# Performance work log

Measured on AMD Instinct MI355X. Metric: run time of the kernel, lower is better.

Reference implementation:

```python
import jax, jax.numpy as jnp
import numpy as np

HEADS = 8
SR = 2
EPS_BN = 1e-5
EPS_LN = 1e-5


def _conv(x, w, b, stride=1, pad=0):
    y = jax.lax.conv_general_dilated(x, w, (stride, stride), [(pad, pad), (pad, pad)],
                                     dimension_numbers=('NCHW', 'OIHW', 'NCHW'))
    return y + b[None, :, None, None]


def _bn(x, g, b):
    # eval-mode BatchNorm with running_mean=0, running_var=1
    return x * (g / jnp.sqrt(1.0 + EPS_BN))[None, :, None, None] + b[None, :, None, None]


def _dwt_haar(x):
    # [B,c,H,W] -> [B,4c,H/2,W/2] stacked as LL,HL,LH,HH (Wave-ViT convention)
    x1 = x[:, :, 0::2, 0::2] / 2
    x2 = x[:, :, 1::2, 0::2] / 2
    x3 = x[:, :, 0::2, 1::2] / 2
    x4 = x[:, :, 1::2, 1::2] / 2
    ll = x1 + x2 + x3 + x4
    hl = -x1 - x2 + x3 + x4
    lh = -x1 + x2 - x3 + x4
    hh = x1 - x2 - x3 + x4
    return jnp.concatenate([ll, hl, lh, hh], axis=1)


def _idwt_haar(y):
    # [B,4c,h,w] -> [B,c,2h,2w], exact inverse of _dwt_haar
    c = y.shape[1] // 4
    ll, hl, lh, hh = y[:, :c], y[:, c:2 * c], y[:, 2 * c:3 * c], y[:, 3 * c:]
    p1 = (ll - hl - lh + hh) / 2  # (0::2, 0::2)
    p2 = (ll - hl + lh - hh) / 2  # (1::2, 0::2)
    p3 = (ll + hl - lh - hh) / 2  # (0::2, 1::2)
    p4 = (ll + hl + lh + hh) / 2  # (1::2, 1::2)
    B, _, h2, w2 = ll.shape
    row0 = jnp.stack([p1, p3], axis=-1)  # even rows
    row1 = jnp.stack([p2, p4], axis=-1)  # odd rows
    out = jnp.stack([row0, row1], axis=3)  # [B,c,h2,2,w2,2]
    return out.reshape(B, c, 2 * h2, 2 * w2)


def setup_inputs() -> dict:
    key = jax.random.key(0)
    ks = jax.random.split(key, 12)
    B, H, W, C = 8, 56, 56, 512
    N = H * W
    c4 = C // 4

    def nrm(k, shp, std):
        return jax.random.normal(k, shp, jnp.float32) * std

    return {
        'x': jax.random.normal(ks[0], (B, N, C), jnp.float32),
        'H': H, 'W': W,
        'reduce_w': nrm(ks[1], (c4, C, 1, 1), (2.0 / c4) ** 0.5),
        'reduce_b': jnp.zeros((c4,), jnp.float32),
        'reduce_g': jnp.ones((c4,), jnp.float32),
        'reduce_beta': jnp.zeros((c4,), jnp.float32),
        'filter_w': nrm(ks[2], (C, C, 3, 3), (2.0 / (9 * C)) ** 0.5),
        'filter_b': jnp.zeros((C,), jnp.float32),
        'filter_g': jnp.ones((C,), jnp.float32),
        'filter_beta': jnp.zeros((C,), jnp.float32),
        'q_w': nrm(ks[3], (C, C), 0.02),
        'q_b': jnp.zeros((C,), jnp.float32),
        'ln_g': jnp.ones((C,), jnp.float32),
        'ln_b': jnp.zeros((C,), jnp.float32),
        'kv_w': nrm(ks[4], (2 * C, C), 0.02),
        'kv_b': jnp.zeros((2 * C,), jnp.float32),
        'kve_w': nrm(ks[5], (C, C, SR, SR), (2.0 / (SR * SR * C)) ** 0.5),
        'kve_b': jnp.zeros((C,), jnp.float32),
        'proj_w': nrm(ks[6], (C, C + c4), 0.02),
        'proj_b': jnp.zeros((C,), jnp.float32),
    }


def reference(x, H, W, reduce_w, reduce_b, reduce_g, reduce_beta,
              filter_w, filter_b, filter_g, filter_beta,
              q_w, q_b, ln_g, ln_b, kv_w, kv_b, kve_w, kve_b, proj_w, proj_b):
    B, N, C = x.shape
    hd = C // HEADS
    scale = hd ** -0.5

    q = (x @ q_w.T + q_b).reshape(B, N, HEADS, hd).transpose(0, 2, 1, 3)  # [B,h,N,d]

    xi = x.reshape(B, H, W, C).transpose(0, 3, 1, 2)  # NCHW
    r = jax.nn.relu(_bn(_conv(xi, reduce_w, reduce_b), reduce_g, reduce_beta))  # [B,C/4,H,W]
    r16 = r.astype(jnp.float16)
    x_dwt = _dwt_haar(r16).astype(jnp.float32)  # [B,C,H/2,W/2]
    x_dwt = jax.nn.relu(_bn(_conv(x_dwt, filter_w, filter_b, pad=1), filter_g, filter_beta))
    x_dwt16 = x_dwt.astype(jnp.float16)
    x_idwt = _idwt_haar(x_dwt16)  # [B,C/4,H,W] fp16
    x_idwt = x_idwt.reshape(B, C // 4, H * W).transpose(0, 2, 1)  # [B,N,C/4]

    x_dwt = x_dwt16.astype(jnp.float32)
    kv_in = _conv(x_dwt, kve_w, kve_b, stride=SR).reshape(B, C, -1).transpose(0, 2, 1)  # [B,M,C]
    mu = kv_in.mean(-1, keepdims=True)
    var = ((kv_in - mu) ** 2).mean(-1, keepdims=True)
    kv_n = (kv_in - mu) / jnp.sqrt(var + EPS_LN) * ln_g + ln_b
    kv = (kv_n @ kv_w.T + kv_b).reshape(B, -1, 2, HEADS, hd).transpose(2, 0, 3, 1, 4)
    k, v = kv[0], kv[1]  # [B,h,M,d]

    attn = jax.nn.softmax(jnp.einsum('bhnd,bhmd->bhnm', q, k) * scale, axis=-1)
    o = jnp.einsum('bhnm,bhmd->bhnd', attn, v).transpose(0, 2, 1, 3).reshape(B, N, C)
    o = jnp.concatenate([o, x_idwt.astype(jnp.float32)], axis=-1)  # [B,N,C+C/4]
    return o @ proj_w.T + proj_b
```

## Files before the change

kernel.cpp:

```cpp
#include <hip/hip_runtime.h>
#include <math.h>


typedef _Float16 half8 __attribute__((ext_vector_type(8)));
typedef float f32x4 __attribute__((ext_vector_type(4)));

static const size_t OFF_X16  = 0;
static const size_t OFF_Q16  = 12845056;
static const size_t OFF_CAT  = 25690112;
static const size_t OFF_R16  = 41746432;
static const size_t OFF_PAD  = 44957696;
static const size_t OFF_DWTB = 48644096;
static const size_t OFF_QRW  = 51855360;
static const size_t OFF_LN16 = 55066624;
static const size_t OFF_KV16 = 55869440;
static const size_t OFF_WT   = 57475072;
static const size_t OFF_KT   = 59834368;
static const size_t OFF_KVW  = 61145088;
static const size_t OFF_PW   = 61669376;
static const size_t OFF_VT   = 62062592;
static const size_t OFF_PART = 62980096;

#define BN_RSQ 0.9999950000374997f
#define SCL2   0.1803368801111204f
#define PART_STRIDE 3211264
#define KVE_STRIDE  802816

__device__ __forceinline__ void async_copy16(const _Float16* g, _Float16* l) {
    __builtin_amdgcn_global_load_lds(
        (const __attribute__((address_space(1))) void*)g,
        (__attribute__((address_space(3))) void*)l, 16, 0, 0);
}

#define WAIT4_BARRIER() asm volatile("s_waitcnt vmcnt(4)\n\ts_barrier" ::: "memory")
#define WAIT0_BARRIER() asm volatile("s_waitcnt vmcnt(0)\n\ts_barrier" ::: "memory")

template <int ALOAD, int EPI>
__global__ __launch_bounds__(256) void gemm16(
    const _Float16* __restrict__ A, const _Float16* __restrict__ W,
    void* __restrict__ outp, int M, int K, int lda, int ldc,
    const float* __restrict__ bias, const float* __restrict__ bng,
    const float* __restrict__ bnb, const float* __restrict__ bias2,
    void* __restrict__ outp2)
{
    __shared__ _Float16 sA[3][128 * 32];
    __shared__ _Float16 sB[3][128 * 32];
    const int t = threadIdx.x;
    const int lane = t & 63, wid = t >> 6;

    int bx = blockIdx.x, by = blockIdx.y;
    {
        int nwg = gridDim.x * gridDim.y;
        if ((nwg & 7) == 0) {
            int orig = by * gridDim.x + bx;
            int cs = nwg >> 3;
            int wg = (orig & 7) * cs + (orig >> 3);
            by = wg % gridDim.y;
            bx = wg / gridDim.y;
        }
    }
    const int m0 = bx * 128, n0 = by * 128;
    const int kbase = blockIdx.z * K;

    const int sr = wid * 16 + (lane >> 2);
    const int sc = (lane & 3) * 8;
    const int stA0 = wid * 512;
    const int stA1 = 2048 + wid * 512;

    const _Float16 *aP0, *aP1;
    if constexpr (ALOAD == 0) {
        int r0 = m0 + sr;      if (r0 > M - 1) r0 = M - 1;
        int r1 = m0 + 64 + sr; if (r1 > M - 1) r1 = M - 1;
        aP0 = A + (size_t)r0 * lda + sc;
        aP1 = A + (size_t)r1 * lda + sc;
    } else {
        int m_ = m0 + sr; if (m_ > M - 1) m_ = M - 1;
        int b_ = m_ / 196, rem = m_ - b_ * 196, i_ = rem / 14, j_ = rem - i_ * 14;
        aP0 = A + ((size_t)(b_ * 784 + 2 * i_ * 28 + 2 * j_)) * 512 + sc;
        m_ = m0 + 64 + sr; if (m_ > M - 1) m_ = M - 1;
        b_ = m_ / 196; rem = m_ - b_ * 196; i_ = rem / 14; j_ = rem - i_ * 14;
        aP1 = A + ((size_t)(b_ * 784 + 2 * i_ * 28 + 2 * j_)) * 512 + sc;
    }
    const int ldw = (ALOAD == 2) ? lda : K;
    const _Float16* bP0 = W + (size_t)(n0 + sr) * ldw + sc;
    const _Float16* bP1 = W + (size_t)(n0 + 64 + sr) * ldw + sc;

    const int mw = wid & 1, nw = wid >> 1;
    const int pAoff = (mw * 64 + (lane & 15)) * 32 + (lane >> 4) * 8;
    const int pBoff = (nw * 64 + (lane & 15)) * 32 + (lane >> 4) * 8;

    f32x4 acc[4][4];
#pragma unroll
    for (int i = 0; i < 4; ++i)
#pragma unroll
        for (int j = 0; j < 4; ++j) acc[i][j] = (f32x4)(0.0f);

    auto aoff_of = [&](int k) -> int {
        if constexpr (ALOAD == 0) {
            return k;
        } else {
            int sub = k >> 9; int ky = sub >> 1, kx = sub & 1;
            return (ky * 28 + kx) * 512 + (k & 511);
        }
    };
    auto stage = [&](int ti, int buf) {
        int k = kbase + ti * 32;
        int aOff = aoff_of(k);
        async_copy16(aP0 + aOff, &sA[buf][stA0]);
        async_copy16(aP1 + aOff, &sA[buf][stA1]);
        async_copy16(bP0 + k, &sB[buf][stA0]);
        async_copy16(bP1 + k, &sB[buf][stA1]);
    };

    const int nt = K >> 5;
    stage(0, 0);
    if (nt > 1) { stage(1, 1); WAIT4_BARRIER(); }
    else        { WAIT0_BARRIER(); }

    int cur = 0;
    for (int i = 0; i < nt; ++i) {
        const _Float16* pA = &sA[cur][0] + pAoff;
        const _Float16* pB = &sB[cur][0] + pBoff;
        half8 aF[4], bF[4];
#pragma unroll
        for (int u = 0; u < 4; ++u) aF[u] = *(const half8*)(pA + u * 512);
#pragma unroll
        for (int u = 0; u < 4; ++u) bF[u] = *(const half8*)(pB + u * 512);

        const bool st = (i + 2 < nt);
        if (st) {
            int nb = cur + 2; if (nb >= 3) nb -= 3;
            stage(i + 2, nb);
        }
#pragma unroll
        for (int u = 0; u < 4; ++u)
#pragma unroll
            for (int j = 0; j < 4; ++j)
                acc[u][j] = __builtin_amdgcn_mfma_f32_16x16x32_f16(
                    aF[u], bF[j], acc[u][j], 0, 0, 0);

        if (i + 1 < nt) {
            if (st) WAIT4_BARRIER();
            else    WAIT0_BARRIER();
        }
        ++cur; if (cur == 3) cur = 0;
    }

    const int orow = m0 + mw * 64 + (lane >> 4) * 4;
    const int ocol = n0 + nw * 64 + (lane & 15);
#pragma unroll
    for (int j = 0; j < 4; ++j) {
        int col = ocol + j * 16;
        float bv = 0.0f, g = 0.0f, b2 = 0.0f;
        if constexpr (EPI == 4) {
            if (n0 >= 512) {
                bv = bias2[col - 512];
                g = bng[col - 512] * BN_RSQ;
                b2 = bnb[col - 512];
            } else {
                bv = bias[col];
            }
        } else if constexpr (EPI != 3) {
            bv = bias[col];
        }
#pragma unroll
        for (int i = 0; i < 4; ++i) {
#pragma unroll
            for (int r = 0; r < 4; ++r) {
                int row = orow + i * 16 + r;
                if (row >= M) continue;
                float v = acc[i][j][r] + bv;
                if constexpr (EPI == 0) {
                    __builtin_nontemporal_store(
                        v, (float*)outp + (size_t)row * ldc + col);
                } else if constexpr (EPI == 3) {
                    ((float*)outp)[(size_t)blockIdx.z * KVE_STRIDE
                                   + (size_t)row * ldc + col] = v;
                } else if constexpr (EPI == 4) {
                    if (n0 >= 512) {
                        v = fmaxf(v * g + b2, 0.0f);
                        ((_Float16*)outp2)[(size_t)row * 128 + (col - 512)] =
                            (_Float16)v;
                    } else {
                        ((_Float16*)outp)[(size_t)row * ldc + col] = (_Float16)v;
                    }
                } else if constexpr (EPI == 5) {
                    if (n0 >= 512) {
                        int hd_ = col - 512;
                        int h_ = hd_ >> 6, d_ = hd_ & 63;
                        int b_ = row / 196, m_ = row - b_ * 196;
                        ((_Float16*)outp2)[((size_t)((b_ * 8 + h_) * 64 + d_)) * 224
                                           + m_] = (_Float16)v;
                    } else {
                        ((_Float16*)outp)[(size_t)row * ldc + col] = (_Float16)v;
                    }
                } else {
                    ((_Float16*)outp)[(size_t)row * ldc + col] = (_Float16)v;
                }
            }
        }
    }
}

__global__ __launch_bounds__(256) void conv_splitk(
    const _Float16* __restrict__ A, const _Float16* __restrict__ W,
    float* __restrict__ partA, float* __restrict__ partB)
{
    __shared__ _Float16 sA[3][128 * 32];
    __shared__ _Float16 sB[3][128 * 32];
    const int t = threadIdx.x;
    const int lane = t & 63, wid = t >> 6;

    int orig = blockIdx.x;
    int wg = (orig & 7) * 98 + (orig >> 3);
    int bx = wg % 49;  int c = wg / 49;
    int by = c & 3,    bz = c >> 2;

    const int m0 = bx * 128, n0 = by * 128;
    const int kbase = bz * 1152;

    const int sr = wid * 16 + (lane >> 2);
    const int sc = (lane & 3) * 8;
    const int stA0 = wid * 512;
    const int stA1 = 2048 + wid * 512;

    int m_ = m0 + sr;
    int b_ = m_ / 784, rem = m_ - b_ * 784, y_ = rem / 28, x_ = rem - y_ * 28;
    const _Float16* aP0 = A + ((size_t)(b_ * 900 + (y_ + 1) * 30 + (x_ + 1))) * 512 + sc;
    m_ = m0 + 64 + sr;
    b_ = m_ / 784; rem = m_ - b_ * 784; y_ = rem / 28; x_ = rem - y_ * 28;
    const _Float16* aP1 = A + ((size_t)(b_ * 900 + (y_ + 1) * 30 + (x_ + 1))) * 512 + sc;
    const _Float16* bP0 = W + (size_t)(n0 + sr) * 4608 + sc;
    const _Float16* bP1 = W + (size_t)(n0 + 64 + sr) * 4608 + sc;

    const int mw = wid & 1, nw = wid >> 1;
    const int pAoff = (mw * 64 + (lane & 15)) * 32 + (lane >> 4) * 8;
    const int pBoff = (nw * 64 + (lane & 15)) * 32 + (lane >> 4) * 8;

    f32x4 acc[4][4];
#pragma unroll
    for (int i = 0; i < 4; ++i)
#pragma unroll
        for (int j = 0; j < 4; ++j) acc[i][j] = (f32x4)(0.0f);

    auto aoff_of = [&](int k) -> int {
        int sub = k >> 9; int s3 = sub / 3;
        int dy = s3 - 1, dx = sub - s3 * 3 - 1;
        return (dy * 30 + dx) * 512 + (k & 511);
    };
    auto stage = [&](int ti, int buf) {
        int k = kbase + ti * 32;
        int aOff = aoff_of(k);
        async_copy16(aP0 + aOff, &sA[buf][stA0]);
        async_copy16(aP1 + aOff, &sA[buf][stA1]);
        async_copy16(bP0 + k, &sB[buf][stA0]);
        async_copy16(bP1 + k, &sB[buf][stA1]);
    };

    const int nt = 36;
    stage(0, 0);
    stage(1, 1);
    WAIT4_BARRIER();

    int cur = 0;
    for (int i = 0; i < nt; ++i) {
        const _Float16* pA = &sA[cur][0] + pAoff;
        const _Float16* pB = &sB[cur][0] + pBoff;
        half8 aF[4], bF[4];
#pragma unroll
        for (int u = 0; u < 4; ++u) aF[u] = *(const half8*)(pA + u * 512);
#pragma unroll
        for (int u = 0; u < 4; ++u) bF[u] = *(const half8*)(pB + u * 512);

        const bool st = (i + 2 < nt);
        if (st) {
            int nb = cur + 2; if (nb >= 3) nb -= 3;
            stage(i + 2, nb);
        }
#pragma unroll
        for (int u = 0; u < 4; ++u)
#pragma unroll
            for (int j = 0; j < 4; ++j)
                acc[u][j] = __builtin_amdgcn_mfma_f32_16x16x32_f16(
                    aF[u], bF[j], acc[u][j], 0, 0, 0);

        if (i + 1 < nt) {
            if (st) WAIT4_BARRIER();
            else    WAIT0_BARRIER();
        }
        ++cur; if (cur == 3) cur = 0;
    }

    float* dst = (bz < 2) ? (partA + (size_t)bz * PART_STRIDE)
                          : (partB + (size_t)(bz - 2) * PART_STRIDE);
    const int orow = m0 + mw * 64 + (lane >> 4) * 4;
    const int ocol = n0 + nw * 64 + (lane & 15);
#pragma unroll
    for (int j = 0; j < 4; ++j) {
#pragma unroll
        for (int i = 0; i < 4; ++i)
#pragma unroll
            for (int r = 0; r < 4; ++r)
                dst[(size_t)(orow + i * 16 + r) * 512 + ocol + j * 16] = acc[i][j][r];
    }
}

__global__ __launch_bounds__(128) void conv_epi_idwt(
    const float* __restrict__ pA, const float* __restrict__ pB,
    _Float16* __restrict__ dwtb, _Float16* __restrict__ cat,
    const float* __restrict__ bias, const float* __restrict__ bng,
    const float* __restrict__ bnb)
{
    int p = blockIdx.x;
    int b = p / 784; int rem = p - b * 784;
    int i = rem / 28;  int j = rem - i * 28;
    int c = threadIdx.x;
    size_t base = (size_t)p * 512;
    _Float16 g16[4];
#pragma unroll
    for (int g = 0; g < 4; ++g) {
        int ch = g * 128 + c;
        float s = (pA[base + ch] + pA[PART_STRIDE + base + ch])
                + (pB[base + ch] + pB[PART_STRIDE + base + ch]);
        float v = (s + bias[ch]) * (bng[ch] * BN_RSQ) + bnb[ch];
        g16[g] = (_Float16)fmaxf(v, 0.0f);
        dwtb[base + ch] = g16[g];
    }
    _Float16 ll = g16[0], hl = g16[1], lh = g16[2], hh = g16[3];
    _Float16 h = (_Float16)0.5f;
    _Float16 p1 = (((ll - hl) - lh) + hh) * h;
    _Float16 p2 = (((ll - hl) + lh) - hh) * h;
    _Float16 p3 = (((ll + hl) - lh) - hh) * h;
    _Float16 p4 = (((ll + hl) + lh) + hh) * h;
    int y = 2 * i, x = 2 * j;
    size_t rb = (size_t)b * 3136;
    __builtin_nontemporal_store(p1, &cat[(rb + (size_t)y * 56 + x) * 640 + 512 + c]);
    __builtin_nontemporal_store(p3, &cat[(rb + (size_t)y * 56 + x + 1) * 640 + 512 + c]);
    __builtin_nontemporal_store(p2, &cat[(rb + (size_t)(y + 1) * 56 + x) * 640 + 512 + c]);
    __builtin_nontemporal_store(p4, &cat[(rb + (size_t)(y + 1) * 56 + x + 1) * 640 + 512 + c]);
}

__device__ __forceinline__ void cvt8_at(
    const float* __restrict__ s, _Float16* __restrict__ d, int i)
{
    const float4* sp = (const float4*)(s + (size_t)i * 8);
    float4 a = sp[0], b = sp[1];
    half8 h;
    h[0] = (_Float16)a.x; h[1] = (_Float16)a.y; h[2] = (_Float16)a.z; h[3] = (_Float16)a.w;
    h[4] = (_Float16)b.x; h[5] = (_Float16)b.y; h[6] = (_Float16)b.z; h[7] = (_Float16)b.w;
    *(half8*)(d + (size_t)i * 8) = h;
}

__global__ __launch_bounds__(256) void prep_kernel(
    const float* __restrict__ qw, const float* __restrict__ rw,
    const float* __restrict__ kvw, const float* __restrict__ pw,
    const float* __restrict__ fw, const float* __restrict__ kw,
    _Float16* __restrict__ qrw16, _Float16* __restrict__ kvw16,
    _Float16* __restrict__ pw16, _Float16* __restrict__ wT,
    _Float16* __restrict__ kT, _Float16* __restrict__ pad,
    _Float16* __restrict__ vt)
{
    int bid = blockIdx.x, tid = threadIdx.x;
    if (bid < 128) {
        cvt8_at(qw, qrw16, bid * 256 + tid);
    } else if (bid < 160) {
        cvt8_at(rw, qrw16 + 262144, (bid - 128) * 256 + tid);
    } else if (bid < 416) {
        cvt8_at(kvw, kvw16, (bid - 160) * 256 + tid);
    } else if (bid < 576) {
        cvt8_at(pw, pw16, (bid - 416) * 256 + tid);
    } else if (bid < 9792) {
        int idx = (bid - 576) * 256 + tid;
        int n = idx / 4608; int r = idx - n * 4608;
        int sub = r >> 9; int ci = r & 511;
        wT[idx] = (_Float16)fw[(size_t)n * 4608 + ci * 9 + sub];
    } else if (bid < 13888) {
        int idx = (bid - 9792) * 256 + tid;
        int n = idx >> 11; int r = idx & 2047;
        int sub = r >> 9; int ci = r & 511;
        kT[idx] = (_Float16)kw[((size_t)n << 11) + (ci << 2) + sub];
    } else if (bid < 15688) {
        int i = (bid - 13888) * 256 + tid;
        *(float4*)(pad + (size_t)i * 8) = make_float4(0.f, 0.f, 0.f, 0.f);
    } else {
        int i = (bid - 15688) * 256 + tid;
        *(float4*)(vt + (size_t)i * 8) = make_float4(0.f, 0.f, 0.f, 0.f);
    }
}

__global__ __launch_bounds__(256) void cvt_f32_f16(
    const float* __restrict__ s, _Float16* __restrict__ d, int n8)
{
    int i = blockIdx.x * 256 + threadIdx.x;
    if (i >= n8) return;
    cvt8_at(s, d, i);
}

__global__ __launch_bounds__(128) void dwt_kernel(
    const _Float16* __restrict__ r, _Float16* __restrict__ pad)
{
    int bid = blockIdx.x;
    int b = bid / 784; int rem = bid - b * 784;
    int i = rem / 28;  int j = rem - i * 28;
    int c = threadIdx.x;
    int y = 2 * i, x = 2 * j;
    size_t base = (size_t)b * 3136;
    _Float16 f1 = r[(base + (size_t)y * 56 + x) * 128 + c];
    _Float16 f2 = r[(base + (size_t)(y + 1) * 56 + x) * 128 + c];
    _Float16 f3 = r[(base + (size_t)y * 56 + (x + 1)) * 128 + c];
    _Float16 f4 = r[(base + (size_t)(y + 1) * 56 + (x + 1)) * 128 + c];
    _Float16 h = (_Float16)0.5f;
    _Float16 x1 = f1 * h, x2 = f2 * h, x3 = f3 * h, x4 = f4 * h;
    _Float16 ll = ((x1 + x2) + x3) + x4;
    _Float16 hl = (((-x1) - x2) + x3) + x4;
    _Float16 lh = (((-x1) + x2) - x3) + x4;
    _Float16 hh = ((x1 - x2) - x3) + x4;
    size_t ob = ((size_t)b * 900 + (size_t)(i + 1) * 30 + (j + 1)) * 512;
    pad[ob + c]       = ll;
    pad[ob + 128 + c] = hl;
    pad[ob + 256 + c] = lh;
    pad[ob + 384 + c] = hh;
}

__global__ __launch_bounds__(256) void ln_kernel(
    const float* __restrict__ part, _Float16* __restrict__ o,
    const float* __restrict__ g, const float* __restrict__ bta,
    const float* __restrict__ kvb)
{
    int wave = threadIdx.x >> 6;
    int lane = threadIdx.x & 63;
    int row = blockIdx.x * 4 + wave;
    int c = lane * 8;
    const float* rp = part + (size_t)row * 512 + c;
    float v[8];
#pragma unroll
    for (int i = 0; i < 8; i += 4) {
        float4 a0 = *(const float4*)(rp + i);
        float4 a1 = *(const float4*)(rp + KVE_STRIDE + i);
        float4 a2 = *(const float4*)(rp + 2 * KVE_STRIDE + i);
        float4 a3 = *(const float4*)(rp + 3 * KVE_STRIDE + i);
        v[i + 0] = (a0.x + a1.x) + (a2.x + a3.x) + kvb[c + i + 0];
        v[i + 1] = (a0.y + a1.y) + (a2.y + a3.y) + kvb[c + i + 1];
        v[i + 2] = (a0.z + a1.z) + (a2.z + a3.z) + kvb[c + i + 2];
        v[i + 3] = (a0.w + a1.w) + (a2.w + a3.w) + kvb[c + i + 3];
    }
    float s = ((v[0] + v[1]) + (v[2] + v[3])) + ((v[4] + v[5]) + (v[6] + v[7]));
#pragma unroll
    for (int off = 32; off; off >>= 1) s += __shfl_xor(s, off);
    float mu = s * (1.0f / 512.0f);
    float sq = 0.0f;
#pragma unroll
    for (int i = 0; i < 8; ++i) { v[i] -= mu; sq += v[i] * v[i]; }
#pragma unroll
    for (int off = 32; off; off >>= 1) sq += __shfl_xor(sq, off);
    float inv = 1.0f / sqrtf(sq * (1.0f / 512.0f) + 1e-5f);
    half8 hv;
#pragma unroll
    for (int i = 0; i < 8; ++i) hv[i] = (_Float16)(v[i] * inv * g[c + i] + bta[c + i]);
    *(half8*)(o + (size_t)row * 512 + c) = hv;
}

__global__ __launch_bounds__(256) void attn_mfma(
    const _Float16* __restrict__ q, const _Float16* __restrict__ kv,
    const _Float16* __restrict__ vt, _Float16* __restrict__ cat)
{
    __shared__ _Float16 sK[64][72];
    __shared__ _Float16 sVT[64][72];
    __shared__ _Float16 sP[4][16][40];
    int bid = blockIdx.x;
    int qt = bid % 49;
    int h  = (bid / 49) & 7;
    int b  = bid / 392;
    int n0 = qt * 64;
    int t = threadIdx.x, lane = t & 63, wid = t >> 6;
    int quad = lane >> 4, l16 = lane & 15;

    const _Float16* qp = q + ((size_t)(b * 3136 + n0 + wid * 16 + l16)) * 512
                           + h * 64 + quad * 8;
    half8 aQ0 = *(const half8*)qp;
    half8 aQ1 = *(const half8*)(qp + 32);

    f32x4 oacc[4];
#pragma unroll
    for (int i = 0; i < 4; ++i) oacc[i] = (f32x4)(0.0f);
    float lsum[4] = {0.f, 0.f, 0.f, 0.f};

    const _Float16* vtb = vt + ((size_t)((b * 8 + h) * 64)) * 224;

    for (int c0 = 0; c0 < 224; c0 += 64) {
        __syncthreads();
#pragma unroll
        for (int it = 0; it < 2; ++it) {
            int slot = t + 256 * it;
            int row = slot >> 3, c8 = (slot & 7) * 8;
            int m = c0 + row; if (m > 195) m = 195;
            *(half8*)&sK[row][c8] =
                *(const half8*)(kv + ((size_t)(b * 196 + m)) * 1024 + h * 64 + c8);
        }
#pragma unroll
        for (int it = 0; it < 2; ++it) {
            int slot = t + 256 * it;
            int row = slot >> 3, c8 = (slot & 7) * 8;
            *(half8*)&sVT[row][c8] =
                *(const half8*)(vtb + (size_t)row * 224 + c0 + c8);
        }
        __syncthreads();

#pragma unroll
        for (int sc = 0; sc < 64; sc += 32) {
            half8 bk00 = *(const half8*)&sK[sc + l16][quad * 8];
            half8 bk01 = *(const half8*)&sK[sc + l16][32 + quad * 8];
            half8 bk10 = *(const half8*)&sK[sc + 16 + l16][quad * 8];
            half8 bk11 = *(const half8*)&sK[sc + 16 + l16][32 + quad * 8];
            f32x4 s0 = (f32x4)(0.0f), s1 = (f32x4)(0.0f);
            s0 = __builtin_amdgcn_mfma_f32_16x16x32_f16(aQ0, bk00, s0, 0, 0, 0);
            s0 = __builtin_amdgcn_mfma_f32_16x16x32_f16(aQ1, bk01, s0, 0, 0, 0);
            s1 = __builtin_amdgcn_mfma_f32_16x16x32_f16(aQ0, bk10, s1, 0, 0, 0);
            s1 = __builtin_amdgcn_mfma_f32_16x16x32_f16(aQ1, bk11, s1, 0, 0, 0);

            int col0 = c0 + sc + l16;
            float msk0 = (col0 < 196) ? 0.0f : -INFINITY;
            float msk1 = (col0 + 16 < 196) ? 0.0f : -INFINITY;
            float p0[4], p1[4];
#pragma unroll
            for (int r = 0; r < 4; ++r) {
                p0[r] = exp2f(s0[r] * SCL2 + msk0);
                p1[r] = exp2f(s1[r] * SCL2 + msk1);
                lsum[r] += p0[r] + p1[r];
            }
#pragma unroll
            for (int r = 0; r < 4; ++r) {
                sP[wid][quad * 4 + r][l16]      = (_Float16)p0[r];
                sP[wid][quad * 4 + r][16 + l16] = (_Float16)p1[r];
            }
            half8 aP = *(const half8*)&sP[wid][l16][quad * 8];
            half8 bv0 = *(const half8*)&sVT[l16][sc + quad * 8];
            half8 bv1 = *(const half8*)&sVT[16 + l16][sc + quad * 8];
            half8 bv2 = *(const half8*)&sVT[32 + l16][sc + quad * 8];
            half8 bv3 = *(const half8*)&sVT[48 + l16][sc + quad * 8];
            oacc[0] = __builtin_amdgcn_mfma_f32_16x16x32_f16(aP, bv0, oacc[0], 0, 0, 0);
            oacc[1] = __builtin_amdgcn_mfma_f32_16x16x32_f16(aP, bv1, oacc[1], 0, 0, 0);
            oacc[2] = __builtin_amdgcn_mfma_f32_16x16x32_f16(aP, bv2, oacc[2], 0, 0, 0);
            oacc[3] = __builtin_amdgcn_mfma_f32_16x16x32_f16(aP, bv3, oacc[3], 0, 0, 0);
        }
    }

    float inv[4];
#pragma unroll
    for (int r = 0; r < 4; ++r) {
        float s = lsum[r];
        s += __shfl_xor(s, 1);
        s += __shfl_xor(s, 2);
        s += __shfl_xor(s, 4);
        s += __shfl_xor(s, 8);
        inv[r] = 1.0f / s;
    }
#pragma unroll
    for (int r = 0; r < 4; ++r) {
        size_t rowoff = ((size_t)(b * 3136 + n0 + wid * 16 + quad * 4 + r)) * 640
                        + h * 64 + l16;
#pragma unroll
        for (int tv = 0; tv < 4; ++tv)
            cat[rowoff + tv * 16] = (_Float16)(oacc[tv][r] * inv[r]);
    }
}

extern "C" void kernel_launch(void* const* d_in, const int* in_sizes, int n_in,
                              void* d_out, int out_size, void* d_ws, size_t ws_size,
                              hipStream_t stream)
{
    const float* x           = (const float*)d_in[0];
    const float* reduce_w    = (const float*)d_in[3];
    const float* reduce_b    = (const float*)d_in[4];
    const float* reduce_g    = (const float*)d_in[5];
    const float* reduce_beta = (const float*)d_in[6];
    const float* filter_w    = (const float*)d_in[7];
    const float* filter_b    = (const float*)d_in[8];
    const float* filter_g    = (const float*)d_in[9];
    const float* filter_beta = (const float*)d_in[10];
    const float* q_w         = (const float*)d_in[11];
    const float* q_b         = (const float*)d_in[12];
    const float* ln_g        = (const float*)d_in[13];
    const float* ln_b        = (const float*)d_in[14];
    const float* kv_w        = (const float*)d_in[15];
    const float* kv_b        = (const float*)d_in[16];
    const float* kve_w       = (const float*)d_in[17];
    const float* kve_b       = (const float*)d_in[18];
    const float* proj_w      = (const float*)d_in[19];
    const float* proj_b      = (const float*)d_in[20];
    float* out = (float*)d_out;
    _Float16* hws = (_Float16*)d_ws;

    _Float16* x16    = hws + OFF_X16;
    _Float16* q16    = hws + OFF_Q16;
    _Float16* cat16  = hws + OFF_CAT;
    _Float16* r16    = hws + OFF_R16;
    _Float16* pad16  = hws + OFF_PAD;
    _Float16* dwtb16 = hws + OFF_DWTB;
    _Float16* qrw16  = hws + OFF_QRW;
    _Float16* ln16   = hws + OFF_LN16;
    _Float16* kv16   = hws + OFF_KV16;
    _Float16* wT16   = hws + OFF_WT;
    _Float16* kT16   = hws + OFF_KT;
    _Float16* kvw16  = hws + OFF_KVW;
    _Float16* pw16   = hws + OFF_PW;
    _Float16* vt16   = hws + OFF_VT;
    float*    partA  = (float*)(hws + OFF_X16);
    float*    partB  = (float*)(hws + OFF_PART);
    float*    kvepart = (float*)(hws + OFF_X16);

    prep_kernel<<<dim3(16136), dim3(256), 0, stream>>>(
        q_w, reduce_w, kv_w, proj_w, filter_w, kve_w,
        qrw16, kvw16, pw16, wT16, kT16, pad16, vt16);

    cvt_f32_f16<<<dim3(6272), dim3(256), 0, stream>>>(x, x16, 1605632);

    gemm16<0, 4><<<dim3(196, 5), dim3(256), 0, stream>>>(
        x16, qrw16, q16, 25088, 512, 512, 512, q_b, reduce_g, reduce_beta,
        reduce_b, r16);

    dwt_kernel<<<dim3(6272), dim3(128), 0, stream>>>(r16, pad16);

    conv_splitk<<<dim3(784), dim3(256), 0, stream>>>(pad16, wT16, partA, partB);

    conv_epi_idwt<<<dim3(6272), dim3(128), 0, stream>>>(
        partA, partB, dwtb16, cat16, filter_b, filter_g, filter_beta);

    gemm16<2, 3><<<dim3(13, 4, 4), dim3(256), 0, stream>>>(
        dwtb16, kT16, kvepart, 1568, 512, 2048, 512, nullptr, nullptr, nullptr,
        nullptr, nullptr);

    ln_kernel<<<dim3(392), dim3(256), 0, stream>>>(kvepart, ln16, ln_g, ln_b, kve_b);

    gemm16<0, 5><<<dim3(13, 8), dim3(256), 0, stream>>>(
        ln16, kvw16, kv16, 1568, 512, 512, 1024, kv_b, nullptr, nullptr,
        nullptr, vt16);

    attn_mfma<<<dim3(3136), dim3(256), 0, stream>>>(q16, kv16, vt16, cat16);

    gemm16<0, 0><<<dim3(196, 4), dim3(256), 0, stream>>>(
        cat16, pw16, out, 25088, 640, 640, 512, proj_b, nullptr, nullptr,
        nullptr, nullptr);
}
```

Measured before the change: 399.0 us.

## Use 256x128 tiles for large GEMMs and conv; fuse x conversion into prep

Adds a gemm16f variant and a conv_splitk_fat kernel that compute 256x128 output tiles per block (8x4 MFMA accumulators per wave) instead of 128x128. The QR, proj GEMMs and the 3x3 conv now run on these, halving grid size and doubling A-tile reuse of each B tile. The f32-to-f16 conversion of x is folded into prep_kernel to save a launch. The larger tiles raise register and LDS use, which can lower occupancy, and leave fewer blocks to fill the GPU (400 for the conv).

```diff
diff --git a/kernel.cpp b/kernel.cpp
--- a/kernel.cpp
+++ b/kernel.cpp
@@ -33,15 +33,14 @@
 }
 
 #define WAIT4_BARRIER() asm volatile("s_waitcnt vmcnt(4)\n\ts_barrier" ::: "memory")
+#define WAIT6_BARRIER() asm volatile("s_waitcnt vmcnt(6)\n\ts_barrier" ::: "memory")
 #define WAIT0_BARRIER() asm volatile("s_waitcnt vmcnt(0)\n\ts_barrier" ::: "memory")
 
 template <int ALOAD, int EPI>
 __global__ __launch_bounds__(256) void gemm16(
     const _Float16* __restrict__ A, const _Float16* __restrict__ W,
     void* __restrict__ outp, int M, int K, int lda, int ldc,
-    const float* __restrict__ bias, const float* __restrict__ bng,
-    const float* __restrict__ bnb, const float* __restrict__ bias2,
-    void* __restrict__ outp2)
+    const float* __restrict__ bias, void* __restrict__ outp2)
 {
     __shared__ _Float16 sA[3][128 * 32];
     __shared__ _Float16 sB[3][128 * 32];
@@ -49,16 +48,6 @@
     const int lane = t & 63, wid = t >> 6;
 
     int bx = blockIdx.x, by = blockIdx.y;
-    {
-        int nwg = gridDim.x * gridDim.y;
-        if ((nwg & 7) == 0) {
-            int orig = by * gridDim.x + bx;
-            int cs = nwg >> 3;
-            int wg = (orig & 7) * cs + (orig >> 3);
-            by = wg % gridDim.y;
-            bx = wg / gridDim.y;
-        }
-    }
     const int m0 = bx * 128, n0 = by * 128;
     const int kbase = blockIdx.z * K;
 
@@ -151,6 +140,131 @@
 #pragma unroll
     for (int j = 0; j < 4; ++j) {
         int col = ocol + j * 16;
+        float bv = 0.0f;
+        if constexpr (EPI == 5) bv = bias[col];
+#pragma unroll
+        for (int i = 0; i < 4; ++i) {
+#pragma unroll
+            for (int r = 0; r < 4; ++r) {
+                int row = orow + i * 16 + r;
+                if (row >= M) continue;
+                float v = acc[i][j][r] + bv;
+                if constexpr (EPI == 3) {
+                    ((float*)outp)[(size_t)blockIdx.z * KVE_STRIDE
+                                   + (size_t)row * ldc + col] = v;
+                } else {
+                    if (n0 >= 512) {
+                        int hd_ = col - 512;
+                        int h_ = hd_ >> 6, d_ = hd_ & 63;
+                        int b_ = row / 196, m_ = row - b_ * 196;
+                        ((_Float16*)outp2)[((size_t)((b_ * 8 + h_) * 64 + d_)) * 224
+                                           + m_] = (_Float16)v;
+                    } else {
+                        ((_Float16*)outp)[(size_t)row * ldc + col] = (_Float16)v;
+                    }
+                }
+            }
+        }
+    }
+}
+
+template <int EPI>
+__global__ __launch_bounds__(256) void gemm16f(
+    const _Float16* __restrict__ A, const _Float16* __restrict__ W,
+    void* __restrict__ outp, int M, int K, int lda, int ldc,
+    const float* __restrict__ bias, const float* __restrict__ bng,
+    const float* __restrict__ bnb, const float* __restrict__ bias2,
+    void* __restrict__ outp2)
+{
+    __shared__ _Float16 sA[3][256 * 32];
+    __shared__ _Float16 sB[3][128 * 32];
+    const int t = threadIdx.x;
+    const int lane = t & 63, wid = t >> 6;
+
+    int bx = blockIdx.x, by = blockIdx.y;
+    {
+        int nwg = gridDim.x * gridDim.y;
+        if ((nwg & 7) == 0) {
+            int orig = by * gridDim.x + bx;
+            int cs = nwg >> 3;
+            int wg = (orig & 7) * cs + (orig >> 3);
+            by = wg % gridDim.y;
+            bx = wg / gridDim.y;
+        }
+    }
+    const int m0 = bx * 256, n0 = by * 128;
+
+    const int sr = wid * 16 + (lane >> 2);
+    const int sc = (lane & 3) * 8;
+    const int stO = wid * 512;
+
+    const _Float16* aP[4];
+#pragma unroll
+    for (int g = 0; g < 4; ++g) {
+        int r_ = m0 + g * 64 + sr; if (r_ > M - 1) r_ = M - 1;
+        aP[g] = A + (size_t)r_ * lda + sc;
+    }
+    const _Float16* bP0 = W + (size_t)(n0 + sr) * K + sc;
+    const _Float16* bP1 = W + (size_t)(n0 + 64 + sr) * K + sc;
+
+    const int mw = wid & 1, nw = wid >> 1;
+    const int pAoff = (mw * 128 + (lane & 15)) * 32 + (lane >> 4) * 8;
+    const int pBoff = (nw * 64 + (lane & 15)) * 32 + (lane >> 4) * 8;
+
+    f32x4 acc[8][4];
+#pragma unroll
+    for (int i = 0; i < 8; ++i)
+#pragma unroll
+        for (int j = 0; j < 4; ++j) acc[i][j] = (f32x4)(0.0f);
+
+    auto stage = [&](int ti, int buf) {
+        int k = ti * 32;
+#pragma unroll
+        for (int g = 0; g < 4; ++g)
+            async_copy16(aP[g] + k, &sA[buf][g * 2048 + stO]);
+        async_copy16(bP0 + k, &sB[buf][stO]);
+        async_copy16(bP1 + k, &sB[buf][2048 + stO]);
+    };
+
+    const int nt = K >> 5;
+    stage(0, 0);
+    stage(1, 1);
+    WAIT6_BARRIER();
+
+    int cur = 0;
+    for (int i = 0; i < nt; ++i) {
+        const _Float16* pA = &sA[cur][0] + pAoff;
+        const _Float16* pB = &sB[cur][0] + pBoff;
+        half8 aF[8], bF[4];
+#pragma unroll
+        for (int u = 0; u < 8; ++u) aF[u] = *(const half8*)(pA + u * 512);
+#pragma unroll
+        for (int u = 0; u < 4; ++u) bF[u] = *(const half8*)(pB + u * 512);
+
+        const bool st = (i + 2 < nt);
+        if (st) {
+            int nb = cur + 2; if (nb >= 3) nb -= 3;
+            stage(i + 2, nb);
+        }
+#pragma unroll
+        for (int u = 0; u < 8; ++u)
+#pragma unroll
+            for (int j = 0; j < 4; ++j)
+                acc[u][j] = __builtin_amdgcn_mfma_f32_16x16x32_f16(
+                    aF[u], bF[j], acc[u][j], 0, 0, 0);
+
+        if (i + 1 < nt) {
+            if (st) WAIT6_BARRIER();
+            else    WAIT0_BARRIER();
+        }
+        ++cur; if (cur == 3) cur = 0;
+    }
+
+    const int orow = m0 + mw * 128 + (lane >> 4) * 4;
+    const int ocol = n0 + nw * 64 + (lane & 15);
+#pragma unroll
+    for (int j = 0; j < 4; ++j) {
+        int col = ocol + j * 16;
         float bv = 0.0f, g = 0.0f, b2 = 0.0f;
         if constexpr (EPI == 4) {
             if (n0 >= 512) {
@@ -160,11 +274,11 @@
             } else {
                 bv = bias[col];
             }
-        } else if constexpr (EPI != 3) {
+        } else {
             bv = bias[col];
         }
 #pragma unroll
-        for (int i = 0; i < 4; ++i) {
+        for (int i = 0; i < 8; ++i) {
 #pragma unroll
             for (int r = 0; r < 4; ++r) {
                 int row = orow + i * 16 + r;
@@ -173,10 +287,7 @@
                 if constexpr (EPI == 0) {
                     __builtin_nontemporal_store(
                         v, (float*)outp + (size_t)row * ldc + col);
-                } else if constexpr (EPI == 3) {
-                    ((float*)outp)[(size_t)blockIdx.z * KVE_STRIDE
-                                   + (size_t)row * ldc + col] = v;
-                } else if constexpr (EPI == 4) {
+                } else {
                     if (n0 >= 512) {
                         v = fmaxf(v * g + b2, 0.0f);
                         ((_Float16*)outp2)[(size_t)row * 128 + (col - 512)] =
@@ -184,62 +295,50 @@
                     } else {
                         ((_Float16*)outp)[(size_t)row * ldc + col] = (_Float16)v;
                     }
-                } else if constexpr (EPI == 5) {
-                    if (n0 >= 512) {
-                        int hd_ = col - 512;
-                        int h_ = hd_ >> 6, d_ = hd_ & 63;
-                        int b_ = row / 196, m_ = row - b_ * 196;
-                        ((_Float16*)outp2)[((size_t)((b_ * 8 + h_) * 64 + d_)) * 224
-                                           + m_] = (_Float16)v;
-                    } else {
-                        ((_Float16*)outp)[(size_t)row * ldc + col] = (_Float16)v;
-                    }
-                } else {
-                    ((_Float16*)outp)[(size_t)row * ldc + col] = (_Float16)v;
                 }
             }
         }
     }
 }
 
-__global__ __launch_bounds__(256) void conv_splitk(
+__global__ __launch_bounds__(256) void conv_splitk_fat(
     const _Float16* __restrict__ A, const _Float16* __restrict__ W,
     float* __restrict__ partA, float* __restrict__ partB)
 {
-    __shared__ _Float16 sA[3][128 * 32];
+    __shared__ _Float16 sA[3][256 * 32];
     __shared__ _Float16 sB[3][128 * 32];
     const int t = threadIdx.x;
     const int lane = t & 63, wid = t >> 6;
 
     int orig = blockIdx.x;
-    int wg = (orig & 7) * 98 + (orig >> 3);
-    int bx = wg % 49;  int c = wg / 49;
+    int wg = (orig & 7) * 50 + (orig >> 3);
+    int bx = wg % 25;  int c = wg / 25;
     int by = c & 3,    bz = c >> 2;
 
-    const int m0 = bx * 128, n0 = by * 128;
+    const int m0 = bx * 256, n0 = by * 128;
     const int kbase = bz * 1152;
 
     const int sr = wid * 16 + (lane >> 2);
     const int sc = (lane & 3) * 8;
-    const int stA0 = wid * 512;
-    const int stA1 = 2048 + wid * 512;
-
-    int m_ = m0 + sr;
-    int b_ = m_ / 784, rem = m_ - b_ * 784, y_ = rem / 28, x_ = rem - y_ * 28;
-    const _Float16* aP0 = A + ((size_t)(b_ * 900 + (y_ + 1) * 30 + (x_ + 1))) * 512 + sc;
-    m_ = m0 + 64 + sr;
-    b_ = m_ / 784; rem = m_ - b_ * 784; y_ = rem / 28; x_ = rem - y_ * 28;
-    const _Float16* aP1 = A + ((size_t)(b_ * 900 + (y_ + 1) * 30 + (x_ + 1))) * 512 + sc;
+    const int stO = wid * 512;
+
+    const _Float16* aP[4];
+#pragma unroll
+    for (int g = 0; g < 4; ++g) {
+        int m_ = m0 + g * 64 + sr; if (m_ > 6271) m_ = 6271;
+        int b_ = m_ / 784, rem = m_ - b_ * 784, y_ = rem / 28, x_ = rem - y_ * 28;
+        aP[g] = A + ((size_t)(b_ * 900 + (y_ + 1) * 30 + (x_ + 1))) * 512 + sc;
+    }
     const _Float16* bP0 = W + (size_t)(n0 + sr) * 4608 + sc;
     const _Float16* bP1 = W + (size_t)(n0 + 64 + sr) * 4608 + sc;
 
     const int mw = wid & 1, nw = wid >> 1;
-    const int pAoff = (mw * 64 + (lane & 15)) * 32 + (lane >> 4) * 8;
+    const int pAoff = (mw * 128 + (lane & 15)) * 32 + (lane >> 4) * 8;
     const int pBoff = (nw * 64 + (lane & 15)) * 32 + (lane >> 4) * 8;
 
-    f32x4 acc[4][4];
-#pragma unroll
-    for (int i = 0; i < 4; ++i)
+    f32x4 acc[8][4];
+#pragma unroll
+    for (int i = 0; i < 8; ++i)
 #pragma unroll
         for (int j = 0; j < 4; ++j) acc[i][j] = (f32x4)(0.0f);
 
@@ -251,24 +350,25 @@
     auto stage = [&](int ti, int buf) {
         int k = kbase + ti * 32;
         int aOff = aoff_of(k);
-        async_copy16(aP0 + aOff, &sA[buf][stA0]);
-        async_copy16(aP1 + aOff, &sA[buf][stA1]);
-        async_copy16(bP0 + k, &sB[buf][stA0]);
-        async_copy16(bP1 + k, &sB[buf][stA1]);
+#pragma unroll
+        for (int g = 0; g < 4; ++g)
+            async_copy16(aP[g] + aOff, &sA[buf][g * 2048 + stO]);
+        async_copy16(bP0 + k, &sB[buf][stO]);
+        async_copy16(bP1 + k, &sB[buf][2048 + stO]);
     };
 
     const int nt = 36;
     stage(0, 0);
     stage(1, 1);
-    WAIT4_BARRIER();
+    WAIT6_BARRIER();
 
     int cur = 0;
     for (int i = 0; i < nt; ++i) {
         const _Float16* pA = &sA[cur][0] + pAoff;
         const _Float16* pB = &sB[cur][0] + pBoff;
-        half8 aF[4], bF[4];
-#pragma unroll
-        for (int u = 0; u < 4; ++u) aF[u] = *(const half8*)(pA + u * 512);
+        half8 aF[8], bF[4];
+#pragma unroll
+        for (int u = 0; u < 8; ++u) aF[u] = *(const half8*)(pA + u * 512);
 #pragma unroll
         for (int u = 0; u < 4; ++u) bF[u] = *(const half8*)(pB + u * 512);
 
@@ -278,14 +378,14 @@
             stage(i + 2, nb);
         }
 #pragma unroll
-        for (int u = 0; u < 4; ++u)
+        for (int u = 0; u < 8; ++u)
 #pragma unroll
             for (int j = 0; j < 4; ++j)
                 acc[u][j] = __builtin_amdgcn_mfma_f32_16x16x32_f16(
                     aF[u], bF[j], acc[u][j], 0, 0, 0);
 
         if (i + 1 < nt) {
-            if (st) WAIT4_BARRIER();
+            if (st) WAIT6_BARRIER();
             else    WAIT0_BARRIER();
         }
         ++cur; if (cur == 3) cur = 0;
@@ -293,15 +393,19 @@
 
     float* dst = (bz < 2) ? (partA + (size_t)bz * PART_STRIDE)
                           : (partB + (size_t)(bz - 2) * PART_STRIDE);
-    const int orow = m0 + mw * 64 + (lane >> 4) * 4;
+    const int orow = m0 + mw * 128 + (lane >> 4) * 4;
     const int ocol = n0 + nw * 64 + (lane & 15);
 #pragma unroll
     for (int j = 0; j < 4; ++j) {
 #pragma unroll
-        for (int i = 0; i < 4; ++i)
-#pragma unroll
-            for (int r = 0; r < 4; ++r)
-                dst[(size_t)(orow + i * 16 + r) * 512 + ocol + j * 16] = acc[i][j][r];
+        for (int i = 0; i < 8; ++i) {
+#pragma unroll
+            for (int r = 0; r < 4; ++r) {
+                int row = orow + i * 16 + r;
+                if (row < 6272)
+                    dst[(size_t)row * 512 + ocol + j * 16] = acc[i][j][r];
+            }
+        }
     }
 }
 
@@ -355,10 +459,11 @@
     const float* __restrict__ qw, const float* __restrict__ rw,
     const float* __restrict__ kvw, const float* __restrict__ pw,
     const float* __restrict__ fw, const float* __restrict__ kw,
+    const float* __restrict__ x,
     _Float16* __restrict__ qrw16, _Float16* __restrict__ kvw16,
     _Float16* __restrict__ pw16, _Float16* __restrict__ wT,
     _Float16* __restrict__ kT, _Float16* __restrict__ pad,
-    _Float16* __restrict__ vt)
+    _Float16* __restrict__ vt, _Float16* __restrict__ x16)
 {
     int bid = blockIdx.x, tid = threadIdx.x;
     if (bid < 128) {
@@ -382,18 +487,12 @@
     } else if (bid < 15688) {
         int i = (bid - 13888) * 256 + tid;
         *(float4*)(pad + (size_t)i * 8) = make_float4(0.f, 0.f, 0.f, 0.f);
-    } else {
+    } else if (bid < 16136) {
         int i = (bid - 15688) * 256 + tid;
         *(float4*)(vt + (size_t)i * 8) = make_float4(0.f, 0.f, 0.f, 0.f);
-    }
-}
-
-__global__ __launch_bounds__(256) void cvt_f32_f16(
-    const float* __restrict__ s, _Float16* __restrict__ d, int n8)
-{
-    int i = blockIdx.x * 256 + threadIdx.x;
-    if (i >= n8) return;
-    cvt8_at(s, d, i);
+    } else {
+        cvt8_at(x, x16, (bid - 16136) * 256 + tid);
+    }
 }
 
 __global__ __launch_bounds__(128) void dwt_kernel(
@@ -609,36 +708,32 @@
     float*    partB  = (float*)(hws + OFF_PART);
     float*    kvepart = (float*)(hws + OFF_X16);
 
-    prep_kernel<<<dim3(16136), dim3(256), 0, stream>>>(
-        q_w, reduce_w, kv_w, proj_w, filter_w, kve_w,
-        qrw16, kvw16, pw16, wT16, kT16, pad16, vt16);
-
-    cvt_f32_f16<<<dim3(6272), dim3(256), 0, stream>>>(x, x16, 1605632);
-
-    gemm16<0, 4><<<dim3(196, 5), dim3(256), 0, stream>>>(
+    prep_kernel<<<dim3(22408), dim3(256), 0, stream>>>(
+        q_w, reduce_w, kv_w, proj_w, filter_w, kve_w, x,
+        qrw16, kvw16, pw16, wT16, kT16, pad16, vt16, x16);
+
+    gemm16f<4><<<dim3(98, 5), dim3(256), 0, stream>>>(
         x16, qrw16, q16, 25088, 512, 512, 512, q_b, reduce_g, reduce_beta,
         reduce_b, r16);
 
     dwt_kernel<<<dim3(6272), dim3(128), 0, stream>>>(r16, pad16);
 
-    conv_splitk<<<dim3(784), dim3(256), 0, stream>>>(pad16, wT16, partA, partB);
+    conv_splitk_fat<<<dim3(400), dim3(256), 0, stream>>>(pad16, wT16, partA, partB);
 
     conv_epi_idwt<<<dim3(6272), dim3(128), 0, stream>>>(
         partA, partB, dwtb16, cat16, filter_b, filter_g, filter_beta);
 
     gemm16<2, 3><<<dim3(13, 4, 4), dim3(256), 0, stream>>>(
-        dwtb16, kT16, kvepart, 1568, 512, 2048, 512, nullptr, nullptr, nullptr,
-        nullptr, nullptr);
+        dwtb16, kT16, kvepart, 1568, 512, 2048, 512, nullptr, nullptr);
 
     ln_kernel<<<dim3(392), dim3(256), 0, stream>>>(kvepart, ln16, ln_g, ln_b, kve_b);
 
     gemm16<0, 5><<<dim3(13, 8), dim3(256), 0, stream>>>(
-        ln16, kvw16, kv16, 1568, 512, 512, 1024, kv_b, nullptr, nullptr,
-        nullptr, vt16);
+        ln16, kvw16, kv16, 1568, 512, 512, 1024, kv_b, vt16);
 
     attn_mfma<<<dim3(3136), dim3(256), 0, stream>>>(q16, kv16, vt16, cat16);
 
-    gemm16<0, 0><<<dim3(196, 4), dim3(256), 0, stream>>>(
+    gemm16f<0><<<dim3(98, 4), dim3(256), 0, stream>>>(
         cat16, pw16, out, 25088, 640, 640, 512, proj_b, nullptr, nullptr,
         nullptr, nullptr);
 }
```

Result: slower. 443.2 us (+11.1%).
